# Optimization experiments

Hardware: AMD Instinct MI355X
Metric: run time of the kernel (lower is better)

## Reference

```python
import jax, jax.numpy as jnp
import numpy as np

N = 50000      # nodes
E = 800000     # edges (before self-loops)
HD = 256       # hidden_dim
H = 4          # heads
C = 64         # per-head channels (hidden_dim // 4)
L = 3          # num_layers
G = 512        # graphs in batch
NEG = 0.2      # LeakyReLU negative slope
EPS = 1e-5     # BatchNorm eps


def setup_inputs() -> dict:
    key = jax.random.key(0)
    ks = jax.random.split(key, 16)
    s_in = 1.0 / np.sqrt(HD)
    inp = {
        "x": jax.random.normal(ks[0], (N, 9), dtype=jnp.float32),
        "edge_index": jax.random.randint(ks[1], (2, E), 0, N, dtype=jnp.int64),
        "edge_attr": jax.random.normal(ks[2], (E, 5), dtype=jnp.float32),
        "batch": jnp.sort(jax.random.randint(ks[3], (N,), 0, G, dtype=jnp.int64)),
        # embeddings
        "Wn": jax.random.normal(ks[4], (9, HD), dtype=jnp.float32) / 3.0,
        "bn_b": jnp.zeros((HD,), jnp.float32),
        "We": jax.random.normal(ks[5], (5, HD), dtype=jnp.float32) / 2.3,
        "be_b": jnp.zeros((HD,), jnp.float32),
        # per-layer GATConv params (stacked over L)
        "lin_w": jax.random.normal(ks[6], (L, HD, H * C), dtype=jnp.float32) * s_in,
        "att_src": jax.random.normal(ks[7], (L, H, C), dtype=jnp.float32) * s_in,
        "att_dst": jax.random.normal(ks[8], (L, H, C), dtype=jnp.float32) * s_in,
        "lin_edge_w": jax.random.normal(ks[9], (L, HD, H * C), dtype=jnp.float32) * s_in,
        "att_edge": jax.random.normal(ks[10], (L, H, C), dtype=jnp.float32) * s_in,
        "conv_bias": jnp.zeros((L, H * C), jnp.float32),
        # BatchNorm affine params (eval mode: running_mean=0, running_var=1)
        "gamma": jnp.ones((L, HD), jnp.float32),
        "beta": jnp.zeros((L, HD), jnp.float32),
    }
    return inp


def _segment_softmax(logits, seg, num):
    m = jax.ops.segment_max(logits, seg, num_segments=num)
    m = jnp.where(jnp.isfinite(m), m, 0.0)
    e = jnp.exp(logits - m[seg])
    s = jax.ops.segment_sum(e, seg, num_segments=num)
    return e / (s[seg] + 1e-16)


def _gat_layer(x, row, col, edge_attr, lin_w, att_s, att_d, lin_e_w, att_e, bias):
    # add self-loops; self-loop edge_attr = mean of incoming edge_attr (PyG fill_value='mean')
    deg = jax.ops.segment_sum(jnp.ones((row.shape[0],), x.dtype), col, num_segments=N)
    loop_attr = jax.ops.segment_sum(edge_attr, col, num_segments=N) / jnp.maximum(deg, 1.0)[:, None]
    sl = jnp.arange(N, dtype=row.dtype)
    r = jnp.concatenate([row, sl])
    c = jnp.concatenate([col, sl])
    ea = jnp.concatenate([edge_attr, loop_attr], axis=0)  # [E+N, HD]

    xh = (x @ lin_w).reshape(N, H, C)                     # [N,H,C]
    a_src = jnp.einsum('nhc,hc->nh', xh, att_s)           # [N,H]
    a_dst = jnp.einsum('nhc,hc->nh', xh, att_d)
    eh = (ea @ lin_e_w).reshape(-1, H, C)                 # [E+N,H,C]
    a_e = jnp.einsum('ehc,hc->eh', eh, att_e)

    alpha = a_src[r] + a_dst[c] + a_e                     # [E+N,H]
    alpha = jnp.where(alpha >= 0, alpha, NEG * alpha)     # leaky_relu
    alpha = _segment_softmax(alpha, c, N)

    msg = xh[r] * alpha[:, :, None]                       # gather + weight
    out = jax.ops.segment_sum(msg, c, num_segments=N)     # scatter-add
    return out.reshape(N, H * C) + bias


def reference(x, edge_index, edge_attr, batch, Wn, bn_b, We, be_b,
              lin_w, att_src, att_dst, lin_edge_w, att_edge, conv_bias,
              gamma, beta):
    row, col = edge_index[0], edge_index[1]
    h = x @ Wn + bn_b                     # node embedding [N,HD]
    ea = edge_attr @ We + be_b            # edge embedding [E,HD]
    inv_std = 1.0 / jnp.sqrt(1.0 + EPS)   # BN eval, running stats (0,1)
    for l in range(L):
        h = _gat_layer(h, row, col, ea, lin_w[l], att_src[l], att_dst[l],
                       lin_edge_w[l], att_edge[l], conv_bias[l])
        h = h * inv_std * gamma[l] + beta[l]
        h = jax.nn.relu(h)                # dropout = identity (eval)
    # global mean pool over graphs
    cnt = jax.ops.segment_sum(jnp.ones((N,), h.dtype), batch, num_segments=G)
    pooled = jax.ops.segment_sum(h, batch, num_segments=G) / jnp.maximum(cnt, 1.0)[:, None]
    return pooled
```

## Files before the change

kernel.cpp:

```cpp
#include <hip/hip_runtime.h>
#include <hip/hip_fp16.h>
#include <math.h>

#define HD 256
#define NHEAD 4
#define CH 64
#define NLAYER 3
#define NEG_SLOPE 0.2f

typedef __attribute__((ext_vector_type(8))) _Float16 half8;
typedef __attribute__((ext_vector_type(4))) _Float16 half4v;
typedef __attribute__((ext_vector_type(4))) float float4v;

__global__ __launch_bounds__(256) void node_embed_kernel(
    const float* __restrict__ x, const float* __restrict__ Wn,
    const float* __restrict__ bn_b, float* __restrict__ h, int N) {
  int base = blockIdx.x * 8;
  int c = threadIdx.x;
  __shared__ float xs[8][9];
  int nn = N - base;
  if (nn > 8) nn = 8;
  if (c < nn * 9) xs[c / 9][c % 9] = x[(size_t)base * 9 + c];
  __syncthreads();
  float b = bn_b[c];
  for (int i = 0; i < nn; ++i) {
    float v = b;
#pragma unroll
    for (int k = 0; k < 9; ++k) v += xs[i][k] * Wn[k * HD + c];
    h[(size_t)(base + i) * HD + c] = v;
  }
}

__global__ __launch_bounds__(256) void precompute_wc_kernel(
    const float* __restrict__ lin_edge_w, const float* __restrict__ att_edge,
    const float* __restrict__ We, const float* __restrict__ be_b,
    float* __restrict__ Wc, float* __restrict__ bc) {
  int lh = blockIdx.x;
  int l = lh >> 2, hh = lh & 3;
  __shared__ float weff[256];
  int j = threadIdx.x;
  const float* lw = lin_edge_w + (size_t)l * HD * HD + (size_t)j * HD + hh * CH;
  const float* ae = att_edge + l * HD + hh * CH;
  float s = 0.f;
#pragma unroll 8
  for (int c = 0; c < CH; ++c) s += lw[c] * ae[c];
  weff[j] = s;
  __syncthreads();
  if (j < 5) {
    float acc = 0.f;
    for (int t = 0; t < 256; ++t) acc += We[j * HD + t] * weff[t];
    Wc[j * 12 + lh] = acc;
  } else if (j == 5) {
    float acc = 0.f;
    for (int t = 0; t < 256; ++t) acc += be_b[t] * weff[t];
    bc[lh] = acc;
  }
}

__global__ __launch_bounds__(64) void conv_bfrag_kernel(
    const float* __restrict__ lin_w, _Float16* __restrict__ Bf_hi) {
  int bid = blockIdx.x;
  int l = bid >> 7;
  int kt = (bid >> 4) & 7, ntg = bid & 15;
  int lane = threadIdx.x;
  const float* B = lin_w + (size_t)l * HD * HD;
  size_t base = ((size_t)bid * 64 + lane) * 8;
  int k0 = kt * 32 + (lane >> 4) * 8;
  int n = ((ntg >= 8) ? 128 : 0) + (lane & 15) * 8 + (ntg & 7);
#pragma unroll
  for (int j = 0; j < 8; ++j) {
    Bf_hi[base + j] = (_Float16)B[(size_t)(k0 + j) * HD + n];
  }
}

__global__ __launch_bounds__(256) void count_deg_kernel(
    const int* __restrict__ col, int* __restrict__ deg, int E) {
  int e = blockIdx.x * 256 + threadIdx.x;
  if (e < E) atomicAdd(&deg[col[e]], 1);
}

__global__ __launch_bounds__(256) void tile_sums_kernel(
    const int* __restrict__ deg, int* __restrict__ tsum, int N) {
  __shared__ int red[256];
  int i = blockIdx.x * 256 + threadIdx.x;
  red[threadIdx.x] = (i < N) ? deg[i] : 0;
  __syncthreads();
  for (int off = 128; off > 0; off >>= 1) {
    if (threadIdx.x < off) red[threadIdx.x] += red[threadIdx.x + off];
    __syncthreads();
  }
  if (threadIdx.x == 0) tsum[blockIdx.x] = red[0];
}

__global__ __launch_bounds__(64) void scan_tsums_kernel(
    const int* __restrict__ tsum, int* __restrict__ toff, int T) {
  int lane = threadIdx.x;
  int carry = 0;
  for (int base = 0; base < T; base += 64) {
    int i = base + lane;
    int orig = (i < T) ? tsum[i] : 0;
    int v = orig;
#pragma unroll
    for (int off = 1; off < 64; off <<= 1) {
      int t = __shfl_up(v, off, 64);
      if (lane >= off) v += t;
    }
    if (i < T) toff[i] = carry + v - orig;
    carry += __shfl(v, 63, 64);
  }
}

__global__ __launch_bounds__(256) void scan_local_kernel(
    const int* __restrict__ deg, const int* __restrict__ toff,
    int* __restrict__ row_start, int N, int E) {
  __shared__ int buf[256];
  int i = blockIdx.x * 256 + threadIdx.x;
  int v = (i < N) ? deg[i] : 0;
  buf[threadIdx.x] = v;
  __syncthreads();
  for (int off = 1; off < 256; off <<= 1) {
    int t = (threadIdx.x >= off) ? buf[threadIdx.x - off] : 0;
    __syncthreads();
    buf[threadIdx.x] += t;
    __syncthreads();
  }
  if (i < N) row_start[i] = toff[blockIdx.x] + buf[threadIdx.x] - v;
  if (blockIdx.x == 0 && threadIdx.x == 0) row_start[N] = E;
}

__global__ __launch_bounds__(256) void scatter_csr_ae_kernel(
    const int* __restrict__ row, const int* __restrict__ col,
    const float* __restrict__ edge_attr, const int* __restrict__ row_start,
    int* __restrict__ cursor, int* __restrict__ rowc,
    const float* __restrict__ Wc, const float* __restrict__ bc,
    float* __restrict__ ae4c_all, int E) {
  __shared__ float sWc[60];
  __shared__ float sbc[12];
  int t = threadIdx.x;
  if (t < 60) sWc[t] = Wc[t];
  if (t < 12) sbc[t] = bc[t];
  __syncthreads();
  int e = blockIdx.x * 256 + t;
  if (e >= E) return;
  int c = col[e];
  int p = atomicAdd(&cursor[c], 1);
  int slot = row_start[c] + p;
  rowc[slot] = row[e];
  float ea[5];
#pragma unroll
  for (int k = 0; k < 5; ++k) ea[k] = edge_attr[(size_t)e * 5 + k];
#pragma unroll
  for (int l = 0; l < NLAYER; ++l) {
    float av[NHEAD];
#pragma unroll
    for (int hh = 0; hh < NHEAD; ++hh) {
      int lh = l * NHEAD + hh;
      float s = sbc[lh];
#pragma unroll
      for (int k = 0; k < 5; ++k) s += ea[k] * sWc[k * 12 + lh];
      av[hh] = s;
    }
    *(float4*)(ae4c_all + ((size_t)l * E + slot) * 4) =
        make_float4(av[0], av[1], av[2], av[3]);
  }
}

__global__ __launch_bounds__(512) void mfma_gemm_fused_kernel(
    const float* __restrict__ A, const _Float16* __restrict__ Bf_hi,
    const float* __restrict__ att_s, const float* __restrict__ att_d,
    __half* __restrict__ xh_h, float* __restrict__ a_src,
    float* __restrict__ a_dst, int N) {
  __shared__ _Float16 sBh[4096];
  const int tid = threadIdx.x;
  const int wave = tid >> 6, lane = tid & 63;
  const int m = lane & 15, quad = lane >> 4;
  const int y = blockIdx.y;
  const int rowbase = blockIdx.x * 128 + wave * 16;
  const int arow = rowbase + m;
  const int arowc = (arow < N) ? arow : (N - 1);

  float4v acc[8];
#pragma unroll
  for (int nt = 0; nt < 8; ++nt) acc[nt] = (float4v){0.f, 0.f, 0.f, 0.f};

  for (int kt = 0; kt < 8; ++kt) {
    __syncthreads();
    {
      const float4* gh = (const float4*)(Bf_hi + ((size_t)kt * 16 + y * 8) * 512);
      ((float4*)sBh)[tid] = gh[tid];
    }
    const float* ap = A + (size_t)arowc * HD + kt * 32 + quad * 8;
    float4 av0 = *(const float4*)(ap);
    float4 av1 = *(const float4*)(ap + 4);
    float af[8] = {av0.x, av0.y, av0.z, av0.w, av1.x, av1.y, av1.z, av1.w};
    half8 ahi, alo;
#pragma unroll
    for (int j = 0; j < 8; ++j) {
      _Float16 hi = (_Float16)af[j];
      ahi[j] = hi;
      alo[j] = (_Float16)(af[j] - (float)hi);
    }
    __syncthreads();
#pragma unroll
    for (int nt = 0; nt < 8; ++nt) {
      half8 bhi = *(const half8*)&sBh[nt * 512 + lane * 8];
      acc[nt] = __builtin_amdgcn_mfma_f32_16x16x32_f16(ahi, bhi, acc[nt], 0, 0, 0);
      acc[nt] = __builtin_amdgcn_mfma_f32_16x16x32_f16(alo, bhi, acc[nt], 0, 0, 0);
    }
  }

  const int hh = y * 2 + (m >> 3);
  const int colbase = y * 128 + m * 8;
  float ats[8], atd[8];
#pragma unroll
  for (int nt = 0; nt < 8; ++nt) {
    ats[nt] = att_s[colbase + nt];
    atd[nt] = att_d[colbase + nt];
  }
  _Float16* xf = (_Float16*)xh_h;
#pragma unroll
  for (int r = 0; r < 4; ++r) {
    int orow = rowbase + quad * 4 + r;
    bool valid = orow < N;
    float ps = 0.f, pd = 0.f;
    half8 h0;
#pragma unroll
    for (int nt = 0; nt < 8; ++nt) {
      h0[nt] = (_Float16)acc[nt][r];
      ps += acc[nt][r] * ats[nt];
      pd += acc[nt][r] * atd[nt];
    }
    if (valid) {
      *(half8*)(xf + (size_t)orow * HD + colbase) = h0;
    }
    ps += __shfl_xor(ps, 1, 64);
    ps += __shfl_xor(ps, 2, 64);
    ps += __shfl_xor(ps, 4, 64);
    pd += __shfl_xor(pd, 1, 64);
    pd += __shfl_xor(pd, 2, 64);
    pd += __shfl_xor(pd, 4, 64);
    if (valid && (m & 7) == 0) {
      a_src[(size_t)orow * NHEAD + hh] = ps;
      a_dst[(size_t)orow * NHEAD + hh] = pd;
    }
  }
}

__global__ __launch_bounds__(256) void fused_aggregate_kernel(
    const __half* __restrict__ xh_h, const int* __restrict__ rowc,
    const int* __restrict__ row_start, const float* __restrict__ ae4c_l,
    const float* __restrict__ a_src, const float* __restrict__ a_dst,
    const float* __restrict__ cb, const float* __restrict__ gm,
    const float* __restrict__ bt, float inv_std, float* __restrict__ hout,
    int N) {
  int tid = threadIdx.x;
  int n = blockIdx.x * 4 + (tid >> 6);
  if (n >= N) return;
  int lane = tid & 63;
  int s = row_start[n], e = row_start[n + 1];

  int hh1 = lane & 3, j = lane >> 2;
  float based1 = a_dst[n * 4 + hh1];
  float m = -3e38f, ssum = 0.f, aes = 0.f;
  for (int i = s + j; i < e; i += 16) {
    int r = rowc[i];
    float ae = ae4c_l[(size_t)i * 4 + hh1];
    float lg = a_src[r * 4 + hh1] + based1 + ae;
    lg = (lg >= 0.f) ? lg : NEG_SLOPE * lg;
    aes += ae;
    float mn = fmaxf(m, lg);
    ssum = ssum * __expf(m - mn) + __expf(lg - mn);
    m = mn;
  }
#pragma unroll
  for (int off = 4; off < 64; off <<= 1) {
    float m2 = __shfl_xor(m, off, 64);
    float s2 = __shfl_xor(ssum, off, 64);
    aes += __shfl_xor(aes, off, 64);
    float mn = fmaxf(m, m2);
    ssum = ssum * __expf(m - mn) + s2 * __expf(m2 - mn);
    m = mn;
  }
  float dinv = (e > s) ? 1.0f / (float)(e - s) : 1.0f;
  float sl = a_src[n * 4 + hh1] + based1 + aes * dinv;
  sl = (sl >= 0.f) ? sl : NEG_SLOPE * sl;
  float mfin = fmaxf(m, sl);
  float self_e = __expf(sl - mfin);
  float tot = ssum * __expf(m - mfin) + self_e;
  float is = 1.0f / (tot + 1e-16f);
  float selfw = self_e * is;

  int hw = lane >> 4;
  float m_h = __shfl(mfin, hw, 64);
  float is_h = __shfl(is, hw, 64);
  float sw_h = __shfl(selfw, hw, 64);
  float based2 = a_dst[n * 4 + hw];

  int eidx = lane & 15;
  int t = lane;
  int ch = t * 4;
  const half4v* xh4 = (const half4v*)xh_h;

  half4v sv = xh4[(size_t)n * 64 + t];
  float a0 = sw_h * (float)sv[0], a1 = sw_h * (float)sv[1];
  float a2 = sw_h * (float)sv[2], a3 = sw_h * (float)sv[3];

  const int base_src = lane & 48;
  for (int chunk = s; chunk < e; chunk += 16) {
    int myedge = chunk + eidx;
    int r_my = 0;
    float w_my = 0.f;
    if (myedge < e) {
      r_my = rowc[myedge];
      float lg = a_src[r_my * 4 + hw] + based2 + ae4c_l[(size_t)myedge * 4 + hw];
      lg = (lg >= 0.f) ? lg : NEG_SLOPE * lg;
      w_my = __expf(lg - m_h) * is_h;
    }
#pragma unroll
    for (int u = 0; u < 16; ++u) {
      float w = __shfl(w_my, base_src + u, 64);
      int ru = __shfl(r_my, base_src + u, 64);
      half4v xv = xh4[(size_t)ru * 64 + t];
      a0 += w * (float)xv[0];
      a1 += w * (float)xv[1];
      a2 += w * (float)xv[2];
      a3 += w * (float)xv[3];
    }
  }
  float4 outv;
  outv.x = fmaxf((a0 + cb[ch + 0]) * inv_std * gm[ch + 0] + bt[ch + 0], 0.f);
  outv.y = fmaxf((a1 + cb[ch + 1]) * inv_std * gm[ch + 1] + bt[ch + 1], 0.f);
  outv.z = fmaxf((a2 + cb[ch + 2]) * inv_std * gm[ch + 2] + bt[ch + 2], 0.f);
  outv.w = fmaxf((a3 + cb[ch + 3]) * inv_std * gm[ch + 3] + bt[ch + 3], 0.f);
  *(float4*)&hout[(size_t)n * HD + ch] = outv;
}

__global__ __launch_bounds__(128) void pool_kernel(
    const float* __restrict__ h, const int* __restrict__ batch,
    float* __restrict__ out, int N) {
  int g = blockIdx.x;
  int ch = blockIdx.y * 128 + threadIdx.x;
  __shared__ int s_lo, s_hi;
  if (threadIdx.x == 0) {
    int lo = 0, hi = N;
    while (lo < hi) { int mid = (lo + hi) >> 1; if (batch[mid] < g) lo = mid + 1; else hi = mid; }
    s_lo = lo;
    lo = 0; hi = N;
    while (lo < hi) { int mid = (lo + hi) >> 1; if (batch[mid] < g + 1) lo = mid + 1; else hi = mid; }
    s_hi = lo;
  }
  __syncthreads();
  int lo = s_lo, hi = s_hi;
  float acc = 0.f;
  for (int n = lo; n < hi; ++n) acc += h[(size_t)n * HD + ch];
  int cnt = hi - lo;
  out[(size_t)g * HD + ch] = acc / (float)(cnt > 0 ? cnt : 1);
}

extern "C" void kernel_launch(void* const* d_in, const int* in_sizes, int n_in,
                              void* d_out, int out_size, void* d_ws, size_t ws_size,
                              hipStream_t stream) {
  const float* x = (const float*)d_in[0];
  const int* ei = (const int*)d_in[1];
  const float* edge_attr = (const float*)d_in[2];
  const int* batch = (const int*)d_in[3];
  const float* Wn = (const float*)d_in[4];
  const float* bn_b = (const float*)d_in[5];
  const float* We = (const float*)d_in[6];
  const float* be_b = (const float*)d_in[7];
  const float* lin_w = (const float*)d_in[8];
  const float* att_src = (const float*)d_in[9];
  const float* att_dst = (const float*)d_in[10];
  const float* lin_edge_w = (const float*)d_in[11];
  const float* att_edge = (const float*)d_in[12];
  const float* conv_bias = (const float*)d_in[13];
  const float* gamma = (const float*)d_in[14];
  const float* beta = (const float*)d_in[15];

  const int N = in_sizes[3];
  const int E = in_sizes[1] / 2;
  const int G = out_size / HD;
  const int* row = ei;
  const int* col = ei + E;

  char* ws = (char*)d_ws;
  size_t off = 0;
  auto alloc = [&](size_t bytes) -> char* {
    char* p = ws + off;
    off += (bytes + 255) & ~(size_t)255;
    return p;
  };
  float* h = (float*)alloc((size_t)N * HD * 4);
  __half* xh_h = (__half*)alloc((size_t)N * HD * 2);
  float* a_src = (float*)alloc((size_t)N * NHEAD * 4);
  float* a_dst = (float*)alloc((size_t)N * NHEAD * 4);
  float* ae4c_all = (float*)alloc((size_t)NLAYER * E * NHEAD * 4);
  int* deg = (int*)alloc((size_t)N * 4);
  int* row_start = (int*)alloc((size_t)(N + 1) * 4);
  int* cursor = (int*)alloc((size_t)N * 4);
  int* rowc = (int*)alloc((size_t)E * 4);
  int* tsum = (int*)alloc(4096);
  int* toff = (int*)alloc(4096);
  float* Wc = (float*)alloc(64 * 4);
  float* bc = (float*)alloc(16 * 4);
  _Float16* Bf_hi = (_Float16*)alloc((size_t)NLAYER * HD * HD * 2);

  hipMemsetAsync(deg, 0, (size_t)N * 4, stream);
  hipMemsetAsync(cursor, 0, (size_t)N * 4, stream);

  node_embed_kernel<<<(N + 7) / 8, 256, 0, stream>>>(x, Wn, bn_b, h, N);
  precompute_wc_kernel<<<12, 256, 0, stream>>>(lin_edge_w, att_edge, We, be_b, Wc, bc);
  conv_bfrag_kernel<<<NLAYER * 128, 64, 0, stream>>>(lin_w, Bf_hi);
  count_deg_kernel<<<(E + 255) / 256, 256, 0, stream>>>(col, deg, E);
  int T = (N + 255) / 256;
  tile_sums_kernel<<<T, 256, 0, stream>>>(deg, tsum, N);
  scan_tsums_kernel<<<1, 64, 0, stream>>>(tsum, toff, T);
  scan_local_kernel<<<T, 256, 0, stream>>>(deg, toff, row_start, N, E);
  scatter_csr_ae_kernel<<<(E + 255) / 256, 256, 0, stream>>>(
      row, col, edge_attr, row_start, cursor, rowc, Wc, bc, ae4c_all, E);

  const float inv_std = 1.0f / sqrtf(1.0f + 1e-5f);
  for (int l = 0; l < NLAYER; ++l) {
    dim3 gg((N + 127) / 128, 2);
    mfma_gemm_fused_kernel<<<gg, 512, 0, stream>>>(
        h, Bf_hi + (size_t)l * HD * HD,
        att_src + l * HD, att_dst + l * HD, xh_h, a_src, a_dst, N);
    fused_aggregate_kernel<<<(N + 3) / 4, 256, 0, stream>>>(
        xh_h, rowc, row_start, ae4c_all + (size_t)l * E * NHEAD, a_src, a_dst,
        conv_bias + l * HD, gamma + l * HD, beta + l * HD, inv_std, h, N);
  }
  dim3 pg(G, 2);
  pool_kernel<<<pg, 128, 0, stream>>>(h, batch, (float*)d_out, N);
}
```

Before: 558.5 us.

## Fuse softmax normalization into single-pass aggregation without max subtraction

Removes the separate edge pass that computed the per-head segment max and sum. Unnormalized exp weights are now accumulated directly during the gather loop, and the sum is normalized at the end, with the self-loop term added afterwards. This avoids re-reading edge indices, edge attention terms and source logits twice per node. Without max subtraction, exp can overflow for large logits, so it relies on logits staying in a safe range.

Result: no change. 564.2 us (+1.0%).

```diff
diff --git a/kernel.cpp b/kernel.cpp
--- a/kernel.cpp
+++ b/kernel.cpp
@@ -259,51 +259,15 @@
   int lane = tid & 63;
   int s = row_start[n], e = row_start[n + 1];
 
-  int hh1 = lane & 3, j = lane >> 2;
-  float based1 = a_dst[n * 4 + hh1];
-  float m = -3e38f, ssum = 0.f, aes = 0.f;
-  for (int i = s + j; i < e; i += 16) {
-    int r = rowc[i];
-    float ae = ae4c_l[(size_t)i * 4 + hh1];
-    float lg = a_src[r * 4 + hh1] + based1 + ae;
-    lg = (lg >= 0.f) ? lg : NEG_SLOPE * lg;
-    aes += ae;
-    float mn = fmaxf(m, lg);
-    ssum = ssum * __expf(m - mn) + __expf(lg - mn);
-    m = mn;
-  }
-#pragma unroll
-  for (int off = 4; off < 64; off <<= 1) {
-    float m2 = __shfl_xor(m, off, 64);
-    float s2 = __shfl_xor(ssum, off, 64);
-    aes += __shfl_xor(aes, off, 64);
-    float mn = fmaxf(m, m2);
-    ssum = ssum * __expf(m - mn) + s2 * __expf(m2 - mn);
-    m = mn;
-  }
-  float dinv = (e > s) ? 1.0f / (float)(e - s) : 1.0f;
-  float sl = a_src[n * 4 + hh1] + based1 + aes * dinv;
-  sl = (sl >= 0.f) ? sl : NEG_SLOPE * sl;
-  float mfin = fmaxf(m, sl);
-  float self_e = __expf(sl - mfin);
-  float tot = ssum * __expf(m - mfin) + self_e;
-  float is = 1.0f / (tot + 1e-16f);
-  float selfw = self_e * is;
-
-  int hw = lane >> 4;
-  float m_h = __shfl(mfin, hw, 64);
-  float is_h = __shfl(is, hw, 64);
-  float sw_h = __shfl(selfw, hw, 64);
-  float based2 = a_dst[n * 4 + hw];
-
-  int eidx = lane & 15;
-  int t = lane;
-  int ch = t * 4;
+  const int hw = lane >> 4;
+  const int eidx = lane & 15;
+  const int t = lane;
+  const int ch = t * 4;
   const half4v* xh4 = (const half4v*)xh_h;
-
-  half4v sv = xh4[(size_t)n * 64 + t];
-  float a0 = sw_h * (float)sv[0], a1 = sw_h * (float)sv[1];
-  float a2 = sw_h * (float)sv[2], a3 = sw_h * (float)sv[3];
+  const float based = a_dst[n * 4 + hw];
+
+  float a0 = 0.f, a1 = 0.f, a2 = 0.f, a3 = 0.f;
+  float zpart = 0.f, aepart = 0.f;
 
   const int base_src = lane & 48;
   for (int chunk = s; chunk < e; chunk += 16) {
@@ -312,9 +276,12 @@
     float w_my = 0.f;
     if (myedge < e) {
       r_my = rowc[myedge];
-      float lg = a_src[r_my * 4 + hw] + based2 + ae4c_l[(size_t)myedge * 4 + hw];
+      float ae = ae4c_l[(size_t)myedge * 4 + hw];
+      float lg = a_src[r_my * 4 + hw] + based + ae;
       lg = (lg >= 0.f) ? lg : NEG_SLOPE * lg;
-      w_my = __expf(lg - m_h) * is_h;
+      w_my = __expf(lg);
+      zpart += w_my;
+      aepart += ae;
     }
 #pragma unroll
     for (int u = 0; u < 16; ++u) {
@@ -327,11 +294,27 @@
       a3 += w * (float)xv[3];
     }
   }
+#pragma unroll
+  for (int off = 1; off < 16; off <<= 1) {
+    zpart += __shfl_xor(zpart, off, 64);
+    aepart += __shfl_xor(aepart, off, 64);
+  }
+  float dinv = (e > s) ? 1.0f / (float)(e - s) : 1.0f;
+  float sl = a_src[n * 4 + hw] + based + aepart * dinv;
+  sl = (sl >= 0.f) ? sl : NEG_SLOPE * sl;
+  float wself = __expf(sl);
+  half4v sv = xh4[(size_t)n * 64 + t];
+  a0 += wself * (float)sv[0];
+  a1 += wself * (float)sv[1];
+  a2 += wself * (float)sv[2];
+  a3 += wself * (float)sv[3];
+  float zinv = 1.0f / (zpart + wself + 1e-16f);
+
   float4 outv;
-  outv.x = fmaxf((a0 + cb[ch + 0]) * inv_std * gm[ch + 0] + bt[ch + 0], 0.f);
-  outv.y = fmaxf((a1 + cb[ch + 1]) * inv_std * gm[ch + 1] + bt[ch + 1], 0.f);
-  outv.z = fmaxf((a2 + cb[ch + 2]) * inv_std * gm[ch + 2] + bt[ch + 2], 0.f);
-  outv.w = fmaxf((a3 + cb[ch + 3]) * inv_std * gm[ch + 3] + bt[ch + 3], 0.f);
+  outv.x = fmaxf((a0 * zinv + cb[ch + 0]) * inv_std * gm[ch + 0] + bt[ch + 0], 0.f);
+  outv.y = fmaxf((a1 * zinv + cb[ch + 1]) * inv_std * gm[ch + 1] + bt[ch + 1], 0.f);
+  outv.z = fmaxf((a2 * zinv + cb[ch + 2]) * inv_std * gm[ch + 2] + bt[ch + 2], 0.f);
+  outv.w = fmaxf((a3 * zinv + cb[ch + 3]) * inv_std * gm[ch + 3] + bt[ch + 3], 0.f);
   *(float4*)&hout[(size_t)n * HD + ch] = outv;
 }
 
```
